# Performance work log

Measured on AMD Instinct MI355X. Metric: run time of the kernel, lower is better.

Reference implementation:

```python
import jax, jax.numpy as jnp
import numpy as np

B, D, E, K = 2048, 768, 8, 2   # tokens, d_model, num_experts, top-k
H = 4 * D                       # FeedForward hidden = 4 * n_embed
LOSS_COEF = 1e-2


def setup_inputs() -> dict:
    key = jax.random.key(0)
    ks = jax.random.split(key, 5)
    s = 0.02
    return {
        "x": jax.random.normal(ks[0], (B, D), jnp.float32),
        "w_gate": jax.random.normal(ks[1], (D, E), jnp.float32) * s,
        "W1": jax.random.normal(ks[2], (E, D, H), jnp.float32) * s,
        "b1": jnp.zeros((E, H), jnp.float32),
        "W2": jax.random.normal(ks[3], (E, H, D), jnp.float32) * s,
        "b2": jnp.zeros((E, D), jnp.float32),
    }


def _cv_squared(v):
    # torch .var() is unbiased (ddof=1)
    eps = 1e-10
    return v.var(ddof=1) / (v.mean() ** 2 + eps)


def reference(x, w_gate, W1, b1, W2, b2):
    # --- noisy_top_k_gating with train=False (clean logits, no noise) ---
    logits = x @ w_gate                                   # [B, E]
    top_vals, top_idx = jax.lax.top_k(logits, K)          # [B, K]
    top_gates = jax.nn.softmax(top_vals, axis=1)          # softmax over the k selected logits
    rows = jnp.arange(x.shape[0])[:, None]
    gates = jnp.zeros_like(logits).at[rows, top_idx].set(top_gates)  # scatter into [B, E]

    importance = gates.sum(0)                             # [E]
    load = (gates > 0).sum(0).astype(jnp.float32)         # [E] (_gates_to_load)
    loss = (_cv_squared(importance) + _cv_squared(load)) * LOSS_COEF

    # --- expert FFNs (dense over experts; gates zero out non-selected) ---
    # equivalent math to SparseDispatcher dispatch/compute/combine:
    # y[b] = sum_e gates[b,e] * FFN_e(x[b])
    h = jax.nn.gelu(jnp.einsum('bd,edh->ebh', x, W1) + b1[:, None, :], approximate=False)  # [E,B,H]
    out = jnp.einsum('ebh,ehd->ebd', h, W2) + b2[:, None, :]                               # [E,B,D]
    y = jnp.einsum('be,ebd->bd', gates, out)                                               # [B,D]
    return y, loss
```

## Files before the change

### kernel.cpp

```cpp
#include <hip/hip_runtime.h>
#include <math.h>

#define Btok 2048
#define Dm   768
#define NE   8
#define Hh   3072
#define OBROWS 5120

typedef short short8 __attribute__((ext_vector_type(8)));
typedef float f32x4  __attribute__((ext_vector_type(4)));

__device__ __forceinline__ short f2bf(float f) {
    unsigned u = __builtin_bit_cast(unsigned, f);
    u += 0x7fffu + ((u >> 16) & 1u);
    return (short)(u >> 16);
}

__device__ __forceinline__ float gelu_exact(float v) {
    float s = v * 0.70710678118654752440f;
    float a = fabsf(s);
    float t = 1.0f / fmaf(0.3275911f, a, 1.0f);
    float p = t * fmaf(t, fmaf(t, fmaf(t, fmaf(t, 1.061405429f, -1.453152027f),
                                       1.421413741f), -0.284496736f), 0.254829592f);
    float er = 1.0f - p * __expf(-s * s);
    er = copysignf(er, s);
    return 0.5f * v * (1.0f + er);
}

#define GLDS(gsrc, ldst)                                                           \
    __builtin_amdgcn_global_load_lds(                                              \
        (const __attribute__((address_space(1))) void*)(gsrc),                     \
        (__attribute__((address_space(3))) void*)(ldst),                           \
        16, 0, 0)

__device__ __forceinline__ void logits_body(const float* __restrict__ x,
                                            const float* __restrict__ wg,
                                            int* __restrict__ t2e,
                                            float* __restrict__ tokgate,
                                            unsigned short* __restrict__ xb,
                                            int b) {
    int wv   = threadIdx.x >> 6;
    int lane = threadIdx.x & 63;
    int tok  = b * 4 + wv;

    const float* xr = x + (size_t)tok * Dm;
    float xv[12];
#pragma unroll
    for (int i = 0; i < 12; ++i) xv[i] = xr[lane + i * 64];

    unsigned short* xw = xb + (size_t)tok * Dm;
#pragma unroll
    for (int i = 0; i < 12; ++i) xw[lane + i * 64] = (unsigned short)f2bf(xv[i]);

    float acc[NE];
#pragma unroll
    for (int e = 0; e < NE; ++e) acc[e] = 0.f;
#pragma unroll
    for (int i = 0; i < 12; ++i) {
        int d = lane + i * 64;
#pragma unroll
        for (int e = 0; e < NE; ++e) acc[e] += xv[i] * wg[d * NE + e];
    }
#pragma unroll
    for (int e = 0; e < NE; ++e) {
#pragma unroll
        for (int off = 32; off > 0; off >>= 1) acc[e] += __shfl_xor(acc[e], off);
    }

    if (lane == 0) {
        int i0 = 0; float v0 = acc[0];
#pragma unroll
        for (int e = 1; e < NE; ++e) { if (acc[e] > v0) { v0 = acc[e]; i0 = e; } }
        int i1 = -1; float v1 = -1e30f;
#pragma unroll
        for (int e = 0; e < NE; ++e) {
            if (e == i0) continue;
            if (acc[e] > v1) { v1 = acc[e]; i1 = e; }
        }
        float tt = __expf(v1 - v0);
        float g0 = 1.0f / (1.0f + tt);
        float g1 = 1.0f - g0;

        t2e[tok * 2 + 0]     = i0;
        t2e[tok * 2 + 1]     = i1;
        tokgate[tok * 2 + 0] = g0;
        tokgate[tok * 2 + 1] = g1;
    }
}

__device__ __forceinline__ void transpose_body(float (*tile)[65],
                                               const float* __restrict__ in,
                                               unsigned short* __restrict__ out,
                                               int ldIn, int ldOut,
                                               size_t eStrideIn, size_t eStrideOut,
                                               int rowOff, int colOff,
                                               int bx, int by, int bz) {
    const float* src = in + (size_t)bz * eStrideIn
                     + (size_t)(rowOff + by * 64) * ldIn + colOff + bx * 64;
    unsigned short* dst = out + (size_t)bz * eStrideOut
                        + (size_t)(bx * 64) * ldOut + by * 64;
    int t = threadIdx.x;
    int r = t >> 4, c4 = (t & 15) * 4;
#pragma unroll
    for (int it = 0; it < 4; ++it) {
        float4 v = *(const float4*)(src + (size_t)(it * 16 + r) * ldIn + c4);
        tile[it * 16 + r][c4 + 0] = v.x;
        tile[it * 16 + r][c4 + 1] = v.y;
        tile[it * 16 + r][c4 + 2] = v.z;
        tile[it * 16 + r][c4 + 3] = v.w;
    }
    __syncthreads();
#pragma unroll
    for (int it = 0; it < 4; ++it) {
        int n = it * 16 + r;
        unsigned short o0 = (unsigned short)f2bf(tile[c4 + 0][n]);
        unsigned short o1 = (unsigned short)f2bf(tile[c4 + 1][n]);
        unsigned short o2 = (unsigned short)f2bf(tile[c4 + 2][n]);
        unsigned short o3 = (unsigned short)f2bf(tile[c4 + 3][n]);
        uint2 o;
        o.x = (unsigned)o0 | ((unsigned)o1 << 16);
        o.y = (unsigned)o2 | ((unsigned)o3 << 16);
        *(uint2*)(dst + (size_t)n * ldOut + c4) = o;
    }
}

__device__ __forceinline__ void transpose_body_1k(float (*tile)[65],
                                                  const float* __restrict__ in,
                                                  unsigned short* __restrict__ out,
                                                  int ldIn, int ldOut,
                                                  size_t eStrideIn, size_t eStrideOut,
                                                  int rowOff, int colOff,
                                                  int bx, int by, int bz) {
    const float* src = in + (size_t)bz * eStrideIn
                     + (size_t)(rowOff + by * 64) * ldIn + colOff + bx * 64;
    unsigned short* dst = out + (size_t)bz * eStrideOut
                        + (size_t)(bx * 64) * ldOut + by * 64;
    int t = threadIdx.x;
    int r = t >> 4, c4 = (t & 15) * 4;
    float4 v = *(const float4*)(src + (size_t)r * ldIn + c4);
    tile[r][c4 + 0] = v.x;
    tile[r][c4 + 1] = v.y;
    tile[r][c4 + 2] = v.z;
    tile[r][c4 + 3] = v.w;
    __syncthreads();
    unsigned short o0 = (unsigned short)f2bf(tile[c4 + 0][r]);
    unsigned short o1 = (unsigned short)f2bf(tile[c4 + 1][r]);
    unsigned short o2 = (unsigned short)f2bf(tile[c4 + 2][r]);
    unsigned short o3 = (unsigned short)f2bf(tile[c4 + 3][r]);
    uint2 o;
    o.x = (unsigned)o0 | ((unsigned)o1 << 16);
    o.y = (unsigned)o2 | ((unsigned)o3 << 16);
    *(uint2*)(dst + (size_t)r * ldOut + c4) = o;
}

__global__ __launch_bounds__(256)
void transpose_kernel(const float* __restrict__ in, unsigned short* __restrict__ out,
                      int ldIn, int ldOut, size_t eStrideIn, size_t eStrideOut,
                      int rowOff, int colOff) {
    __shared__ float tile[64][65];
    transpose_body(tile, in, out, ldIn, ldOut, eStrideIn, eStrideOut, rowOff, colOff,
                   blockIdx.x, blockIdx.y, blockIdx.z);
}

__global__ __launch_bounds__(256)
void prep_kernel(const float* __restrict__ x,
                 const float* __restrict__ wg,
                 int* __restrict__ t2e,
                 float* __restrict__ tokgate,
                 unsigned short* __restrict__ xb,
                 const float* __restrict__ W1, unsigned short* __restrict__ w1t,
                 int Hc, int colBase) {
    __shared__ float tile[64][65];
    int b = blockIdx.x;
    const int NL = Btok / 4;

    if (b < NL) {
        logits_body(x, wg, t2e, tokgate, xb, b);
    } else {
        int nx1 = Hc / 64, ny1 = Dm / 64;
        int q  = b - NL;
        int bx = q % nx1; q /= nx1;
        int by = q % ny1;
        int bz = q / ny1;
        transpose_body(tile, W1, w1t, Hh, Dm, (size_t)Dm * Hh, (size_t)Hc * Dm,
                       0, colBase, bx, by, bz);
    }
}

__global__ __launch_bounds__(1024)
void assign_kernel(const int* __restrict__ t2e,
                   const float* __restrict__ tokgate,
                   int* __restrict__ padded,
                   int* __restrict__ offsets,
                   int* __restrict__ list,
                   int* __restrict__ tokes,
                   float* __restrict__ loss_out,
                   const float* __restrict__ W2,
                   unsigned short* __restrict__ w2t,
                   int Hc) {
    __shared__ int   scnt[NE];
    __shared__ int   spad[NE];
    __shared__ float simp[NE];
    __shared__ float tile[64][65];

    if (blockIdx.x > 0) {
        int ti = blockIdx.x - 1;
        int nx2 = Dm / 64, ny2 = Hc / 64;
        int bx = ti % nx2; int q = ti / nx2;
        int by = q % ny2;
        int bz = q / ny2;
        transpose_body_1k(tile, W2, w2t, Dm, Hc, (size_t)Hh * Dm, (size_t)Dm * Hc,
                          0, 0, bx, by, bz);
        return;
    }

    int tid = threadIdx.x;
    if (tid < NE) { scnt[tid] = 0; simp[tid] = 0.f; }
    __syncthreads();

#pragma unroll
    for (int it = 0; it < Btok / 1024; ++it) {
        int tok = tid + it * 1024;
        int e0 = t2e[tok * 2], e1 = t2e[tok * 2 + 1];
        float g0 = tokgate[tok * 2], g1 = tokgate[tok * 2 + 1];
        int s0 = atomicAdd(&scnt[e0], 1);
        int s1 = atomicAdd(&scnt[e1], 1);
        list[e0 * Btok + s0] = tok;
        list[e1 * Btok + s1] = tok;
        tokes[tok * 2 + 0] = (e0 << 13) | s0;
        tokes[tok * 2 + 1] = (e1 << 13) | s1;
        atomicAdd(&simp[e0], g0);
        atomicAdd(&simp[e1], g1);
    }
    __syncthreads();

    if (tid == 0) {
        int off = 0;
        for (int e = 0; e < NE; ++e) {
            int p = (scnt[e] + 127) & ~127;
            spad[e]    = p;
            padded[e]  = p;
            offsets[e] = off;
            off += p;
        }
        float mi = 0.f, ml = 0.f;
        for (int e = 0; e < NE; ++e) { mi += simp[e]; ml += (float)scnt[e]; }
        mi *= (1.0f / NE); ml *= (1.0f / NE);
        float vi = 0.f, vl = 0.f;
        for (int e = 0; e < NE; ++e) {
            float di = simp[e] - mi;        vi += di * di;
            float dl = (float)scnt[e] - ml; vl += dl * dl;
        }
        vi /= (NE - 1); vl /= (NE - 1);
        loss_out[0] = 1e-2f * (vi / (mi * mi + 1e-10f) + vl / (ml * ml + 1e-10f));
    }
    __syncthreads();

    for (int e = 0; e < NE; ++e) {
        int c = scnt[e], p = spad[e];
        for (int s = c + tid; s < p; s += 1024) list[e * Btok + s] = 0;
    }
}

__global__ __launch_bounds__(256)
void gemm1_kernel(const unsigned short* __restrict__ xb,
                  const unsigned short* __restrict__ w1t,
                  const float* __restrict__ b1,
                  const int* __restrict__ list,
                  const int* __restrict__ padded,
                  const int* __restrict__ offsets,
                  unsigned short* __restrict__ hbuf,
                  int Hc, int colBase, int nG1, int nTr, int tixBase,
                  const float* __restrict__ W2,
                  unsigned short* __restrict__ w2t) {
    __shared__ union __align__(16) {
        struct { unsigned short As[2][4096]; unsigned short Bs[2][4096]; } g;
        float tile[64][65];
    } sm;

    int b = blockIdx.x;
    int gid;
    if (nTr > 0) {
        int total = nG1 + nTr;
        int tc  = (int)(((long long)b * nTr) / total);
        int tc1 = (int)(((long long)(b + 1) * nTr) / total);
        if (tc1 != tc) {
            int tix = tixBase + tc;
            int nx2 = Dm / 64, ny2 = Hc / 64;
            int bx = tix % nx2; int q = tix / nx2;
            int by = q % ny2;
            int bz = q / ny2;
            transpose_body(sm.tile, W2, w2t, Dm, Hc, (size_t)Hh * Dm, (size_t)Dm * Hc,
                           0, 0, bx, by, bz);
            return;
        }
        gid = b - tc;
    } else {
        gid = b;
    }

    int NTQ = Hc / 128;
    int nt = gid % NTQ;
    int mt = (gid / NTQ) % 16;
    int e  = gid / (NTQ * 16);
    if (mt * 128 >= padded[e]) return;
    int roff = offsets[e];

    int t = threadIdx.x, w = t >> 6, lane = t & 63;
    int lr = lane & 15, lh = lane >> 4;
    int wr = (w >> 1) * 64, wc = (w & 1) * 64;
    int r0 = t >> 2;
    int ce = ((t & 3) ^ ((r0 >> 1) & 3)) * 8;
    int ks = (lh ^ ((lr >> 1) & 3)) * 8;

    const int* lst = list + e * Btok + mt * 128;
    int tok0 = lst[r0], tok1 = lst[64 + r0];
    const unsigned short* pa0 = xb + (size_t)tok0 * Dm + ce;
    const unsigned short* pa1 = xb + (size_t)tok1 * Dm + ce;
    const unsigned short* wbp = w1t + ((size_t)e * Hc + (size_t)nt * 128) * Dm;
    const unsigned short* pb0 = wbp + (size_t)r0 * Dm + ce;
    const unsigned short* pb1 = wbp + (size_t)(64 + r0) * Dm + ce;

    int s0 = __builtin_amdgcn_readfirstlane(w * 1024);

    f32x4 acc[4][4];
#pragma unroll
    for (int i = 0; i < 4; ++i)
#pragma unroll
        for (int j = 0; j < 4; ++j) acc[i][j] = (f32x4){0.f, 0.f, 0.f, 0.f};

    auto stage = [&](int buf, int kb) {
        GLDS(pa0 + kb, (char*)&sm.g.As[buf][0] + s0);
        GLDS(pa1 + kb, (char*)&sm.g.As[buf][0] + s0 + 4096);
        GLDS(pb0 + kb, (char*)&sm.g.Bs[buf][0] + s0);
        GLDS(pb1 + kb, (char*)&sm.g.Bs[buf][0] + s0 + 4096);
    };
    auto compute = [&](int buf) {
        short8 a[4], bq[4];
#pragma unroll
        for (int i = 0; i < 4; ++i) a[i] = *(const short8*)&sm.g.As[buf][(wr + i * 16 + lr) * 32 + ks];
#pragma unroll
        for (int j = 0; j < 4; ++j) bq[j] = *(const short8*)&sm.g.Bs[buf][(wc + j * 16 + lr) * 32 + ks];
#pragma unroll
        for (int i = 0; i < 4; ++i)
#pragma unroll
            for (int j = 0; j < 4; ++j)
                acc[i][j] = __builtin_amdgcn_mfma_f32_16x16x32_bf16(a[i], bq[j], acc[i][j], 0, 0, 0);
    };

    const int NTK = Dm / 32;
    stage(0, 0);
    __syncthreads();
    int cur = 0;
    for (int kt = 0; kt < NTK; ++kt) {
        if (kt + 1 < NTK) stage(cur ^ 1, (kt + 1) * 32);
        compute(cur);
        __syncthreads();
        cur ^= 1;
    }

    float bj[4];
#pragma unroll
    for (int j = 0; j < 4; ++j)
        bj[j] = b1[(size_t)e * Hh + colBase + nt * 128 + wc + j * 16 + lr];
#pragma unroll
    for (int i = 0; i < 4; ++i) {
#pragma unroll
        for (int j = 0; j < 4; ++j) {
#pragma unroll
            for (int r = 0; r < 4; ++r) {
                int row = wr + i * 16 + lh * 4 + r;
                float v = acc[i][j][r] + bj[j];
                v = gelu_exact(v);
                hbuf[(size_t)(roff + mt * 128 + row) * Hc + nt * 128 + wc + j * 16 + lr]
                    = (unsigned short)f2bf(v);
            }
        }
    }
}

__global__ __launch_bounds__(256)
void gemm2_kernel(const unsigned short* __restrict__ hbuf,
                  const unsigned short* __restrict__ w2t,
                  const int* __restrict__ padded,
                  const int* __restrict__ offsets,
                  float* __restrict__ obuf,
                  int Hc, int MT, int accum) {
    int id = blockIdx.x;
    int e  = id & 7;
    int rr = id >> 3;
    int mt = rr % MT; rr /= MT;
    int nt = rr % 6;
    int sk = rr / 6;
    if (mt * 128 >= padded[e]) return;
    int roff = offsets[e];
    int Kc = Hc >> 1, K0 = sk * Kc;

    __shared__ unsigned short As[2][4096];
    __shared__ unsigned short Bs[2][4096];

    int t = threadIdx.x, w = t >> 6, lane = t & 63;
    int lr = lane & 15, lh = lane >> 4;
    int wr = (w >> 1) * 64, wc = (w & 1) * 64;
    int r0 = t >> 2;
    int ce = ((t & 3) ^ ((r0 >> 1) & 3)) * 8;
    int ks = (lh ^ ((lr >> 1) & 3)) * 8;

    const unsigned short* ab  = hbuf + (size_t)(roff + mt * 128) * Hc + K0;
    const unsigned short* pa0 = ab + (size_t)r0 * Hc + ce;
    const unsigned short* pa1 = ab + (size_t)(64 + r0) * Hc + ce;
    const unsigned short* wbp = w2t + ((size_t)e * Dm + (size_t)nt * 128) * Hc + K0;
    const unsigned short* pb0 = wbp + (size_t)r0 * Hc + ce;
    const unsigned short* pb1 = wbp + (size_t)(64 + r0) * Hc + ce;

    int s0 = __builtin_amdgcn_readfirstlane(w * 1024);

    f32x4 acc[4][4];
#pragma unroll
    for (int i = 0; i < 4; ++i)
#pragma unroll
        for (int j = 0; j < 4; ++j) acc[i][j] = (f32x4){0.f, 0.f, 0.f, 0.f};

    auto stage = [&](int buf, int kb) {
        GLDS(pa0 + kb, (char*)&As[buf][0] + s0);
        GLDS(pa1 + kb, (char*)&As[buf][0] + s0 + 4096);
        GLDS(pb0 + kb, (char*)&Bs[buf][0] + s0);
        GLDS(pb1 + kb, (char*)&Bs[buf][0] + s0 + 4096);
    };
    auto compute = [&](int buf) {
        short8 a[4], bq[4];
#pragma unroll
        for (int i = 0; i < 4; ++i) a[i] = *(const short8*)&As[buf][(wr + i * 16 + lr) * 32 + ks];
#pragma unroll
        for (int j = 0; j < 4; ++j) bq[j] = *(const short8*)&Bs[buf][(wc + j * 16 + lr) * 32 + ks];
#pragma unroll
        for (int i = 0; i < 4; ++i)
#pragma unroll
            for (int j = 0; j < 4; ++j)
                acc[i][j] = __builtin_amdgcn_mfma_f32_16x16x32_bf16(a[i], bq[j], acc[i][j], 0, 0, 0);
    };

    const int NTK = Kc / 32;
    stage(0, 0);
    __syncthreads();
    int cur = 0;
    for (int kt = 0; kt < NTK; ++kt) {
        if (kt + 1 < NTK) stage(cur ^ 1, (kt + 1) * 32);
        compute(cur);
        __syncthreads();
        cur ^= 1;
    }

    float* orow = obuf + (size_t)sk * OBROWS * Dm
                + (size_t)(roff + mt * 128) * Dm + nt * 128;
#pragma unroll
    for (int i = 0; i < 4; ++i) {
#pragma unroll
        for (int r = 0; r < 4; ++r) {
            int row = wr + i * 16 + lh * 4 + r;
#pragma unroll
            for (int j = 0; j < 4; ++j) {
                int col = wc + j * 16 + lr;
                float v = acc[i][j][r];
                if (accum) v += orow[(size_t)row * Dm + col];
                orow[(size_t)row * Dm + col] = v;
            }
        }
    }
}

__global__ __launch_bounds__(256)
void combine_kernel(const float* __restrict__ obuf,
                    const int* __restrict__ offsets,
                    const int* __restrict__ tokes,
                    const float* __restrict__ tokgate,
                    const float* __restrict__ b2,
                    float* __restrict__ y) {
    int wv = threadIdx.x >> 6, lane = threadIdx.x & 63;
    int tok = blockIdx.x * 4 + wv;
    int p0 = tokes[tok * 2], p1 = tokes[tok * 2 + 1];
    float g0 = tokgate[tok * 2], g1 = tokgate[tok * 2 + 1];
    int e0 = p0 >> 13, ss0 = p0 & 8191;
    int e1 = p1 >> 13, ss1 = p1 & 8191;
    size_t r0 = (size_t)(offsets[e0] + ss0) * Dm;
    size_t r1 = (size_t)(offsets[e1] + ss1) * Dm;
    const size_t SLAB = (size_t)OBROWS * Dm;
#pragma unroll
    for (int i = 0; i < 3; ++i) {
        int col = (lane + i * 64) * 4;
        float4 a0 = *(const float4*)(obuf + r0 + col);
        float4 a1 = *(const float4*)(obuf + SLAB + r0 + col);
        float4 c0 = *(const float4*)(obuf + r1 + col);
        float4 c1 = *(const float4*)(obuf + SLAB + r1 + col);
        float4 be0 = *(const float4*)(b2 + (size_t)e0 * Dm + col);
        float4 be1 = *(const float4*)(b2 + (size_t)e1 * Dm + col);
        float4 o;
        o.x = g0 * (a0.x + a1.x + be0.x) + g1 * (c0.x + c1.x + be1.x);
        o.y = g0 * (a0.y + a1.y + be0.y) + g1 * (c0.y + c1.y + be1.y);
        o.z = g0 * (a0.z + a1.z + be0.z) + g1 * (c0.z + c1.z + be1.z);
        o.w = g0 * (a0.w + a1.w + be0.w) + g1 * (c0.w + c1.w + be1.w);
        *(float4*)(y + (size_t)tok * Dm + col) = o;
    }
}

extern "C" void kernel_launch(void* const* d_in, const int* in_sizes, int n_in,
                              void* d_out, int out_size, void* d_ws, size_t ws_size,
                              hipStream_t stream) {
    const float* x  = (const float*)d_in[0];
    const float* wg = (const float*)d_in[1];
    const float* W1 = (const float*)d_in[2];
    const float* b1 = (const float*)d_in[3];
    const float* W2 = (const float*)d_in[4];
    const float* b2 = (const float*)d_in[5];
    float* y = (float*)d_out;

    char* ws = (char*)d_ws;
    int*   padded     = (int*)(ws + 32);
    int*   offsets    = (int*)(ws + 64);
    int*   list       = (int*)(ws + 1024);
    int*   tokes      = (int*)(ws + 132096);
    float* tokgate    = (float*)(ws + 148480);
    int*   t2e        = (int*)(ws + 164864);
    unsigned short* xb = (unsigned short*)(ws + 262144);

    size_t base = (size_t)4 << 20;
    size_t osz  = (size_t)2 * OBROWS * Dm * sizeof(float);
    int C = 8;
    size_t wsz = 0, hsz = 0;
    for (int c = 1; c <= 8; c <<= 1) {
        wsz = (size_t)NE * (Hh / c) * Dm * 2;
        hsz = (size_t)OBROWS * (Hh / c) * 2;
        size_t need = base + 2 * wsz + hsz + ((c == 1) ? 0 : osz);
        C = c;
        if (need <= ws_size) break;
    }
    int Hc = Hh / C;
    wsz = (size_t)NE * Hc * Dm * 2;
    hsz = (size_t)OBROWS * Hc * 2;
    unsigned short* w1t  = (unsigned short*)(ws + base);
    unsigned short* w2t  = (unsigned short*)(ws + base + wsz);
    unsigned short* hbuf = (unsigned short*)(ws + base + 2 * wsz);
    float* obuf = (C == 1) ? (float*)w1t : (float*)(ws + base + 2 * wsz + hsz);

    const int MT = 16;
    int nT1 = (Hc / 64) * (Dm / 64) * NE;
    int nT2 = (Dm / 64) * (Hc / 64) * NE;
    int nG1 = (Hc / 128) * MT * NE;

    int nTa = (nT2 < 2048) ? nT2 : 2048;
    int nTr = nT2 - nTa;

    prep_kernel<<<Btok / 4 + nT1, 256, 0, stream>>>(
        x, wg, t2e, tokgate, xb, W1, w1t, Hc, 0);
    assign_kernel<<<1 + nTa, 1024, 0, stream>>>(t2e, tokgate, padded, offsets, list, tokes,
                                                y + (size_t)Btok * Dm, W2, w2t, Hc);

    for (int c = 0; c < C; ++c) {
        if (c > 0) {
            transpose_kernel<<<dim3(Hc / 64, Dm / 64, NE), 256, 0, stream>>>(
                W1, w1t, Hh, Dm, (size_t)Dm * Hh, (size_t)Hc * Dm, 0, c * Hc);
            transpose_kernel<<<dim3(Dm / 64, Hc / 64, NE), 256, 0, stream>>>(
                W2, w2t, Dm, Hc, (size_t)Hh * Dm, (size_t)Dm * Hc, c * Hc, 0);
        }
        int extra = (c == 0) ? nTr : 0;
        gemm1_kernel<<<nG1 + extra, 256, 0, stream>>>(
            xb, w1t, b1, list, padded, offsets, hbuf, Hc, c * Hc, nG1, extra, nTa, W2, w2t);
        gemm2_kernel<<<8 * MT * 6 * 2, 256, 0, stream>>>(
            hbuf, w2t, padded, offsets, obuf, Hc, MT, (c == 0) ? 0 : 1);
    }
    combine_kernel<<<Btok / 4, 256, 0, stream>>>(obuf, offsets, tokes, tokgate, b2, y);
}
```

Baseline: 132.9 us.

## Fuse expert combine into GEMM2 epilogue with gated atomic scatter-add

Measured after the change: 142.7 us. +7.3%, slower.

```diff
diff --git a/kernel.cpp b/kernel.cpp
--- a/kernel.cpp
+++ b/kernel.cpp
@@ -5,7 +5,6 @@
 #define Dm   768
 #define NE   8
 #define Hh   3072
-#define OBROWS 5120
 
 typedef short short8 __attribute__((ext_vector_type(8)));
 typedef float f32x4  __attribute__((ext_vector_type(4)));
@@ -192,8 +191,9 @@
                    const float* __restrict__ tokgate,
                    int* __restrict__ padded,
                    int* __restrict__ offsets,
+                   int* __restrict__ counts,
                    int* __restrict__ list,
-                   int* __restrict__ tokes,
+                   float* __restrict__ gslot,
                    float* __restrict__ loss_out,
                    const float* __restrict__ W2,
                    unsigned short* __restrict__ w2t,
@@ -227,8 +227,8 @@
         int s1 = atomicAdd(&scnt[e1], 1);
         list[e0 * Btok + s0] = tok;
         list[e1 * Btok + s1] = tok;
-        tokes[tok * 2 + 0] = (e0 << 13) | s0;
-        tokes[tok * 2 + 1] = (e1 << 13) | s1;
+        gslot[e0 * Btok + s0] = g0;
+        gslot[e1 * Btok + s1] = g1;
         atomicAdd(&simp[e0], g0);
         atomicAdd(&simp[e1], g1);
     }
@@ -241,6 +241,7 @@
             spad[e]    = p;
             padded[e]  = p;
             offsets[e] = off;
+            counts[e]  = scnt[e];
             off += p;
         }
         float mi = 0.f, ml = 0.f;
@@ -384,8 +385,12 @@
                   const unsigned short* __restrict__ w2t,
                   const int* __restrict__ padded,
                   const int* __restrict__ offsets,
-                  float* __restrict__ obuf,
-                  int Hc, int MT, int accum) {
+                  const int* __restrict__ counts,
+                  const int* __restrict__ list,
+                  const float* __restrict__ gslot,
+                  const float* __restrict__ b2,
+                  float* __restrict__ y,
+                  int Hc, int MT, int firstChunk) {
     int id = blockIdx.x;
     int e  = id & 7;
     int rr = id >> 3;
@@ -451,55 +456,30 @@
         cur ^= 1;
     }
 
-    float* orow = obuf + (size_t)sk * OBROWS * Dm
-                + (size_t)(roff + mt * 128) * Dm + nt * 128;
+    int addb2 = (firstChunk && sk == 0) ? 1 : 0;
+    int cnt = counts[e];
+    const int*   lst = list  + e * Btok + mt * 128;
+    const float* gsl = gslot + e * Btok + mt * 128;
+    float bcol[4];
+#pragma unroll
+    for (int j = 0; j < 4; ++j)
+        bcol[j] = addb2 ? b2[(size_t)e * Dm + nt * 128 + wc + j * 16 + lr] : 0.f;
+
 #pragma unroll
     for (int i = 0; i < 4; ++i) {
 #pragma unroll
         for (int r = 0; r < 4; ++r) {
             int row = wr + i * 16 + lh * 4 + r;
+            if (mt * 128 + row >= cnt) continue;
+            int   tok = lst[row];
+            float g   = gsl[row];
+            float* yr = y + (size_t)tok * Dm + nt * 128;
 #pragma unroll
             for (int j = 0; j < 4; ++j) {
                 int col = wc + j * 16 + lr;
-                float v = acc[i][j][r];
-                if (accum) v += orow[(size_t)row * Dm + col];
-                orow[(size_t)row * Dm + col] = v;
+                atomicAdd(&yr[col], g * (acc[i][j][r] + bcol[j]));
             }
         }
-    }
-}
-
-__global__ __launch_bounds__(256)
-void combine_kernel(const float* __restrict__ obuf,
-                    const int* __restrict__ offsets,
-                    const int* __restrict__ tokes,
-                    const float* __restrict__ tokgate,
-                    const float* __restrict__ b2,
-                    float* __restrict__ y) {
-    int wv = threadIdx.x >> 6, lane = threadIdx.x & 63;
-    int tok = blockIdx.x * 4 + wv;
-    int p0 = tokes[tok * 2], p1 = tokes[tok * 2 + 1];
-    float g0 = tokgate[tok * 2], g1 = tokgate[tok * 2 + 1];
-    int e0 = p0 >> 13, ss0 = p0 & 8191;
-    int e1 = p1 >> 13, ss1 = p1 & 8191;
-    size_t r0 = (size_t)(offsets[e0] + ss0) * Dm;
-    size_t r1 = (size_t)(offsets[e1] + ss1) * Dm;
-    const size_t SLAB = (size_t)OBROWS * Dm;
-#pragma unroll
-    for (int i = 0; i < 3; ++i) {
-        int col = (lane + i * 64) * 4;
-        float4 a0 = *(const float4*)(obuf + r0 + col);
-        float4 a1 = *(const float4*)(obuf + SLAB + r0 + col);
-        float4 c0 = *(const float4*)(obuf + r1 + col);
-        float4 c1 = *(const float4*)(obuf + SLAB + r1 + col);
-        float4 be0 = *(const float4*)(b2 + (size_t)e0 * Dm + col);
-        float4 be1 = *(const float4*)(b2 + (size_t)e1 * Dm + col);
-        float4 o;
-        o.x = g0 * (a0.x + a1.x + be0.x) + g1 * (c0.x + c1.x + be1.x);
-        o.y = g0 * (a0.y + a1.y + be0.y) + g1 * (c0.y + c1.y + be1.y);
-        o.z = g0 * (a0.z + a1.z + be0.z) + g1 * (c0.z + c1.z + be1.z);
-        o.w = g0 * (a0.w + a1.w + be0.w) + g1 * (c0.w + c1.w + be1.w);
-        *(float4*)(y + (size_t)tok * Dm + col) = o;
     }
 }
 
@@ -514,33 +494,33 @@
     const float* b2 = (const float*)d_in[5];
     float* y = (float*)d_out;
 
+    hipMemsetAsync(y, 0, (size_t)Btok * Dm * sizeof(float), stream);
+
     char* ws = (char*)d_ws;
     int*   padded     = (int*)(ws + 32);
     int*   offsets    = (int*)(ws + 64);
+    int*   counts     = (int*)(ws + 96);
     int*   list       = (int*)(ws + 1024);
-    int*   tokes      = (int*)(ws + 132096);
     float* tokgate    = (float*)(ws + 148480);
     int*   t2e        = (int*)(ws + 164864);
+    float* gslot      = (float*)(ws + 184320);
     unsigned short* xb = (unsigned short*)(ws + 262144);
 
     size_t base = (size_t)4 << 20;
-    size_t osz  = (size_t)2 * OBROWS * Dm * sizeof(float);
     int C = 8;
     size_t wsz = 0, hsz = 0;
     for (int c = 1; c <= 8; c <<= 1) {
         wsz = (size_t)NE * (Hh / c) * Dm * 2;
-        hsz = (size_t)OBROWS * (Hh / c) * 2;
-        size_t need = base + 2 * wsz + hsz + ((c == 1) ? 0 : osz);
+        hsz = (size_t)(Btok * 2 + NE * 128) * (Hh / c) * 2;
+        size_t need = base + 2 * wsz + hsz;
         C = c;
         if (need <= ws_size) break;
     }
     int Hc = Hh / C;
     wsz = (size_t)NE * Hc * Dm * 2;
-    hsz = (size_t)OBROWS * Hc * 2;
     unsigned short* w1t  = (unsigned short*)(ws + base);
     unsigned short* w2t  = (unsigned short*)(ws + base + wsz);
     unsigned short* hbuf = (unsigned short*)(ws + base + 2 * wsz);
-    float* obuf = (C == 1) ? (float*)w1t : (float*)(ws + base + 2 * wsz + hsz);
 
     const int MT = 16;
     int nT1 = (Hc / 64) * (Dm / 64) * NE;
@@ -552,8 +532,9 @@
 
     prep_kernel<<<Btok / 4 + nT1, 256, 0, stream>>>(
         x, wg, t2e, tokgate, xb, W1, w1t, Hc, 0);
-    assign_kernel<<<1 + nTa, 1024, 0, stream>>>(t2e, tokgate, padded, offsets, list, tokes,
-                                                y + (size_t)Btok * Dm, W2, w2t, Hc);
+    assign_kernel<<<1 + nTa, 1024, 0, stream>>>(t2e, tokgate, padded, offsets, counts,
+                                                list, gslot, y + (size_t)Btok * Dm,
+                                                W2, w2t, Hc);
 
     for (int c = 0; c < C; ++c) {
         if (c > 0) {
@@ -566,7 +547,6 @@
         gemm1_kernel<<<nG1 + extra, 256, 0, stream>>>(
             xb, w1t, b1, list, padded, offsets, hbuf, Hc, c * Hc, nG1, extra, nTa, W2, w2t);
         gemm2_kernel<<<8 * MT * 6 * 2, 256, 0, stream>>>(
-            hbuf, w2t, padded, offsets, obuf, Hc, MT, (c == 0) ? 0 : 1);
-    }
-    combine_kernel<<<Btok / 4, 256, 0, stream>>>(obuf, offsets, tokes, tokgate, b2, y);
-}
+            hbuf, w2t, padded, offsets, counts, list, gslot, b2, y, Hc, MT, (c == 0) ? 1 : 0);
+    }
+}
```

## Widen gemm1 tile to 128x256 with 512 threads and cap chunk count at four

Applied to the files above, without the earlier changes.

After: 168.2 us. 1.27x slower.

```diff
diff --git a/kernel.cpp b/kernel.cpp
--- a/kernel.cpp
+++ b/kernel.cpp
@@ -113,6 +113,42 @@
 #pragma unroll
     for (int it = 0; it < 4; ++it) {
         int n = it * 16 + r;
+        unsigned short o0 = (unsigned short)f2bf(tile[c4 + 0][n]);
+        unsigned short o1 = (unsigned short)f2bf(tile[c4 + 1][n]);
+        unsigned short o2 = (unsigned short)f2bf(tile[c4 + 2][n]);
+        unsigned short o3 = (unsigned short)f2bf(tile[c4 + 3][n]);
+        uint2 o;
+        o.x = (unsigned)o0 | ((unsigned)o1 << 16);
+        o.y = (unsigned)o2 | ((unsigned)o3 << 16);
+        *(uint2*)(dst + (size_t)n * ldOut + c4) = o;
+    }
+}
+
+__device__ __forceinline__ void transpose_body_512(float (*tile)[65],
+                                                   const float* __restrict__ in,
+                                                   unsigned short* __restrict__ out,
+                                                   int ldIn, int ldOut,
+                                                   size_t eStrideIn, size_t eStrideOut,
+                                                   int rowOff, int colOff,
+                                                   int bx, int by, int bz) {
+    const float* src = in + (size_t)bz * eStrideIn
+                     + (size_t)(rowOff + by * 64) * ldIn + colOff + bx * 64;
+    unsigned short* dst = out + (size_t)bz * eStrideOut
+                        + (size_t)(bx * 64) * ldOut + by * 64;
+    int t = threadIdx.x;
+    int r = t >> 4, c4 = (t & 15) * 4;
+#pragma unroll
+    for (int it = 0; it < 2; ++it) {
+        float4 v = *(const float4*)(src + (size_t)(it * 32 + r) * ldIn + c4);
+        tile[it * 32 + r][c4 + 0] = v.x;
+        tile[it * 32 + r][c4 + 1] = v.y;
+        tile[it * 32 + r][c4 + 2] = v.z;
+        tile[it * 32 + r][c4 + 3] = v.w;
+    }
+    __syncthreads();
+#pragma unroll
+    for (int it = 0; it < 2; ++it) {
+        int n = it * 32 + r;
         unsigned short o0 = (unsigned short)f2bf(tile[c4 + 0][n]);
         unsigned short o1 = (unsigned short)f2bf(tile[c4 + 1][n]);
         unsigned short o2 = (unsigned short)f2bf(tile[c4 + 2][n]);
@@ -262,7 +298,7 @@
     }
 }
 
-__global__ __launch_bounds__(256)
+__global__ __launch_bounds__(512)
 void gemm1_kernel(const unsigned short* __restrict__ xb,
                   const unsigned short* __restrict__ w1t,
                   const float* __restrict__ b1,
@@ -274,7 +310,7 @@
                   const float* __restrict__ W2,
                   unsigned short* __restrict__ w2t) {
     __shared__ union __align__(16) {
-        struct { unsigned short As[2][4096]; unsigned short Bs[2][4096]; } g;
+        struct { unsigned short As[2][4096]; unsigned short Bs[2][8192]; } g;
         float tile[64][65];
     } sm;
 
@@ -290,8 +326,8 @@
             int bx = tix % nx2; int q = tix / nx2;
             int by = q % ny2;
             int bz = q / ny2;
-            transpose_body(sm.tile, W2, w2t, Dm, Hc, (size_t)Hh * Dm, (size_t)Dm * Hc,
-                           0, 0, bx, by, bz);
+            transpose_body_512(sm.tile, W2, w2t, Dm, Hc, (size_t)Hh * Dm, (size_t)Dm * Hc,
+                               0, 0, bx, by, bz);
             return;
         }
         gid = b - tc;
@@ -299,7 +335,7 @@
         gid = b;
     }
 
-    int NTQ = Hc / 128;
+    int NTQ = Hc / 256;
     int nt = gid % NTQ;
     int mt = (gid / NTQ) % 16;
     int e  = gid / (NTQ * 16);
@@ -308,18 +344,18 @@
 
     int t = threadIdx.x, w = t >> 6, lane = t & 63;
     int lr = lane & 15, lh = lane >> 4;
-    int wr = (w >> 1) * 64, wc = (w & 1) * 64;
+    int wr = (w & 1) * 64;
+    int wc = (w >> 1) * 64;
     int r0 = t >> 2;
     int ce = ((t & 3) ^ ((r0 >> 1) & 3)) * 8;
     int ks = (lh ^ ((lr >> 1) & 3)) * 8;
 
     const int* lst = list + e * Btok + mt * 128;
-    int tok0 = lst[r0], tok1 = lst[64 + r0];
+    int tok0 = lst[r0];
     const unsigned short* pa0 = xb + (size_t)tok0 * Dm + ce;
-    const unsigned short* pa1 = xb + (size_t)tok1 * Dm + ce;
-    const unsigned short* wbp = w1t + ((size_t)e * Hc + (size_t)nt * 128) * Dm;
+    const unsigned short* wbp = w1t + ((size_t)e * Hc + (size_t)nt * 256) * Dm;
     const unsigned short* pb0 = wbp + (size_t)r0 * Dm + ce;
-    const unsigned short* pb1 = wbp + (size_t)(64 + r0) * Dm + ce;
+    const unsigned short* pb1 = wbp + (size_t)(128 + r0) * Dm + ce;
 
     int s0 = __builtin_amdgcn_readfirstlane(w * 1024);
 
@@ -331,9 +367,8 @@
 
     auto stage = [&](int buf, int kb) {
         GLDS(pa0 + kb, (char*)&sm.g.As[buf][0] + s0);
-        GLDS(pa1 + kb, (char*)&sm.g.As[buf][0] + s0 + 4096);
         GLDS(pb0 + kb, (char*)&sm.g.Bs[buf][0] + s0);
-        GLDS(pb1 + kb, (char*)&sm.g.Bs[buf][0] + s0 + 4096);
+        GLDS(pb1 + kb, (char*)&sm.g.Bs[buf][0] + s0 + 8192);
     };
     auto compute = [&](int buf) {
         short8 a[4], bq[4];
@@ -362,7 +397,7 @@
     float bj[4];
 #pragma unroll
     for (int j = 0; j < 4; ++j)
-        bj[j] = b1[(size_t)e * Hh + colBase + nt * 128 + wc + j * 16 + lr];
+        bj[j] = b1[(size_t)e * Hh + colBase + nt * 256 + wc + j * 16 + lr];
 #pragma unroll
     for (int i = 0; i < 4; ++i) {
 #pragma unroll
@@ -372,7 +407,7 @@
                 int row = wr + i * 16 + lh * 4 + r;
                 float v = acc[i][j][r] + bj[j];
                 v = gelu_exact(v);
-                hbuf[(size_t)(roff + mt * 128 + row) * Hc + nt * 128 + wc + j * 16 + lr]
+                hbuf[(size_t)(roff + mt * 128 + row) * Hc + nt * 256 + wc + j * 16 + lr]
                     = (unsigned short)f2bf(v);
             }
         }
@@ -525,9 +560,9 @@
 
     size_t base = (size_t)4 << 20;
     size_t osz  = (size_t)2 * OBROWS * Dm * sizeof(float);
-    int C = 8;
+    int C = 4;
     size_t wsz = 0, hsz = 0;
-    for (int c = 1; c <= 8; c <<= 1) {
+    for (int c = 1; c <= 4; c <<= 1) {
         wsz = (size_t)NE * (Hh / c) * Dm * 2;
         hsz = (size_t)OBROWS * (Hh / c) * 2;
         size_t need = base + 2 * wsz + hsz + ((c == 1) ? 0 : osz);
@@ -545,7 +580,7 @@
     const int MT = 16;
     int nT1 = (Hc / 64) * (Dm / 64) * NE;
     int nT2 = (Dm / 64) * (Hc / 64) * NE;
-    int nG1 = (Hc / 128) * MT * NE;
+    int nG1 = (Hc / 256) * MT * NE;
 
     int nTa = (nT2 < 2048) ? nT2 : 2048;
     int nTr = nT2 - nTa;
@@ -563,7 +598,7 @@
                 W2, w2t, Dm, Hc, (size_t)Hh * Dm, (size_t)Dm * Hc, c * Hc, 0);
         }
         int extra = (c == 0) ? nTr : 0;
-        gemm1_kernel<<<nG1 + extra, 256, 0, stream>>>(
+        gemm1_kernel<<<nG1 + extra, 512, 0, stream>>>(
             xb, w1t, b1, list, padded, offsets, hbuf, Hc, c * Hc, nG1, extra, nTa, W2, w2t);
         gemm2_kernel<<<8 * MT * 6 * 2, 256, 0, stream>>>(
             hbuf, w2t, padded, offsets, obuf, Hc, MT, (c == 0) ? 0 : 1);
```
